# Kernel tuning notes

Hardware: AMD Instinct MI355X
Metric: run time of the kernel (lower is better)

Reference implementation:

```python
import jax, jax.numpy as jnp
import numpy as np

B, T, D, HD = 4, 4096, 1024, 64

def setup_inputs() -> dict:
    key = jax.random.key(0)
    k1, k2, k3, k4 = jax.random.split(key, 4)
    scale = 1.0 / np.sqrt(D)
    return {
        "x": jax.random.normal(k1, (B, T, D), dtype=jnp.float32),
        "Wq": jax.random.normal(k2, (HD, D), dtype=jnp.float32) * scale,
        "Wk": jax.random.normal(k3, (HD, D), dtype=jnp.float32) * scale,
        "Wv": jax.random.normal(k4, (HD, D), dtype=jnp.float32) * scale,
    }

def reference(x, Wq, Wk, Wv):
    # x: [B,T,D]; W*: [head_dim, D] (torch Linear weight layout)
    Q = jnp.einsum('btd,hd->bth', x, Wq)  # [B,T,HD]
    K = jnp.einsum('btd,hd->bth', x, Wk)
    V = jnp.einsum('btd,hd->bth', x, Wv)
    hd = Q.shape[-1]
    scores = jnp.einsum('bqh,bkh->bqk', Q, K) * (hd ** -0.5)  # [B,T,T]
    t = scores.shape[1]
    causal = jnp.tril(jnp.ones((t, t), dtype=bool))
    scores = jnp.where(causal, scores, -jnp.inf)
    att = jax.nn.softmax(scores, axis=-1)
    return jnp.einsum('bqk,bkh->bqh', att, V)  # [B,T,HD]
```

## Files before the change

### kernel.cpp

```cpp
#include <hip/hip_runtime.h>
#include <stdint.h>

#define B_  4
#define T_  4096
#define D_  1024
#define HD_ 64
#define BT_ 16384

typedef short bf16x8 __attribute__((ext_vector_type(8)));
typedef float f32x4  __attribute__((ext_vector_type(4)));
typedef float f32x16 __attribute__((ext_vector_type(16)));
typedef unsigned short u16;
typedef u16 u16x4 __attribute__((ext_vector_type(4)));
typedef unsigned int u32;
typedef u32 u32x4 __attribute__((ext_vector_type(4)));

#define M0L2_  11.54156032f
#define QSCALE_ 0.18033688f

#define CPB_   132
#define NSLOT_ (4 * CPB_ * 2)

__device__ __forceinline__ u16 f2bf(float f) {
    union { float f; unsigned u; } v; v.f = f;
    unsigned r = (v.u + 0x7FFF + ((v.u >> 16) & 1)) >> 16;
    return (u16)r;
}
__device__ __forceinline__ float bf2f(u16 u) {
    union { unsigned u; float f; } v; v.u = ((unsigned)u) << 16;
    return v.f;
}
__device__ __forceinline__ u32 cvt_pk_bf16(float lo, float hi) {
    u32 r;
    asm("v_cvt_pk_bf16_f32 %0, %1, %2" : "=v"(r) : "v"(lo), "v"(hi));
    return r;
}

__global__ __launch_bounds__(256) void wconv_kernel(
    const float* __restrict__ wq, const float* __restrict__ wk,
    const float* __restrict__ wv, u16* __restrict__ wb)
{
    const int j   = blockIdx.x >> 5;
    const int off = (blockIdx.x & 31) * 2048 + threadIdx.x * 8;
    const float* src = (j == 0) ? wq : ((j == 1) ? wk : wv);
    f32x4 a0 = *(const f32x4*)(src + off);
    f32x4 a1 = *(const f32x4*)(src + off + 4);
    u32x4 b;
    b[0] = cvt_pk_bf16(a0[0], a0[1]);
    b[1] = cvt_pk_bf16(a0[2], a0[3]);
    b[2] = cvt_pk_bf16(a1[0], a1[1]);
    b[3] = cvt_pk_bf16(a1[2], a1[3]);
    *(u32x4*)(wb + j * 65536 + off) = b;
}

struct StageSet { f32x4 xa, xb; bf16x8 w0, w1, w2; };

__global__ __launch_bounds__(512, 2) void qkv_kernel(
    const float* __restrict__ x, const u16* __restrict__ wb,
    u16* __restrict__ qs, u16* __restrict__ kss, u16* __restrict__ vssT)
{
    __shared__ __align__(16) u16 xt[2][64][72];
    __shared__ __align__(16) u16 wt[2][192][72];

    const int tid  = threadIdx.x;
    const int lane = tid & 63;
    const int w    = tid >> 6;
    const int quad = lane >> 4;
    const int l16  = lane & 15;
    const int row0 = blockIdx.x * 64;
    const int rh   = w >> 2;
    const int ct   = w & 3;

    const int xrow = tid >> 3;
    const int xcg  = tid & 7;

    f32x4 acc[2][3];
    #pragma unroll
    for (int s = 0; s < 2; ++s)
        #pragma unroll
        for (int g = 0; g < 3; ++g) acc[s][g] = (f32x4)0.0f;

    const float* xbase = x + (size_t)(row0 + xrow) * D_ + xcg * 8;

    auto load_tile = [&](StageSet& S, int t) {
        const float* xp = xbase + t * 64;
        S.xa = *(const f32x4*)xp; S.xb = *(const f32x4*)(xp + 4);
        const u16* wp = wb + t * 64;
        S.w0 = *(const bf16x8*)(wp + (size_t)((tid       ) >> 3) * D_ + ((tid       ) & 7) * 8);
        S.w1 = *(const bf16x8*)(wp + (size_t)((tid +  512) >> 3) * D_ + ((tid +  512) & 7) * 8);
        S.w2 = *(const bf16x8*)(wp + (size_t)((tid + 1024) >> 3) * D_ + ((tid + 1024) & 7) * 8);
    };
    auto store_tile = [&](const StageSet& S, int bufi) {
        u32x4 px;
        px[0] = cvt_pk_bf16(S.xa[0], S.xa[1]);
        px[1] = cvt_pk_bf16(S.xa[2], S.xa[3]);
        px[2] = cvt_pk_bf16(S.xb[0], S.xb[1]);
        px[3] = cvt_pk_bf16(S.xb[2], S.xb[3]);
        *(u32x4*)&xt[bufi][xrow][xcg * 8] = px;
        *(bf16x8*)&wt[bufi][(tid       ) >> 3][((tid       ) & 7) * 8] = S.w0;
        *(bf16x8*)&wt[bufi][(tid +  512) >> 3][((tid +  512) & 7) * 8] = S.w1;
        *(bf16x8*)&wt[bufi][(tid + 1024) >> 3][((tid + 1024) & 7) * 8] = S.w2;
    };
    auto compute = [&](int bufi) {
        #pragma unroll
        for (int ks = 0; ks < 2; ++ks) {
            bf16x8 a[2];
            #pragma unroll
            for (int s = 0; s < 2; ++s)
                a[s] = *(const bf16x8*)&xt[bufi][rh * 32 + s * 16 + l16][ks * 32 + quad * 8];
            #pragma unroll
            for (int g = 0; g < 3; ++g) {
                bf16x8 bfr = *(const bf16x8*)&wt[bufi][(ct * 3 + g) * 16 + l16][ks * 32 + quad * 8];
                #pragma unroll
                for (int s = 0; s < 2; ++s)
                    acc[s][g] = __builtin_amdgcn_mfma_f32_16x16x32_bf16(a[s], bfr, acc[s][g], 0, 0, 0);
            }
        }
    };

    StageSet A, B;
    load_tile(A, 0);
    load_tile(B, 1);
    store_tile(A, 0);
    __syncthreads();

    #pragma unroll
    for (int kc2 = 0; kc2 < 8; ++kc2) {
        const int kc = kc2 * 2;
        if (kc + 2 < 16) load_tile(A, kc + 2);
        compute(0);
        store_tile(B, 1);
        __syncthreads();
        if (kc + 3 < 16) load_tile(B, kc + 3);
        compute(1);
        if (kc + 2 < 16) store_tile(A, 0);
        __syncthreads();
    }

    #pragma unroll
    for (int s = 0; s < 2; ++s) {
        #pragma unroll
        for (int g = 0; g < 3; ++g) {
            const int n = (ct * 3 + g) * 16 + l16;
            const int j = n >> 6, h = n & 63;
            const int rbase = row0 + rh * 32 + s * 16 + quad * 4;
            if (j == 0) {
                #pragma unroll
                for (int r = 0; r < 4; ++r) qs[(size_t)(rbase + r) * HD_ + h] = f2bf(acc[s][g][r] * QSCALE_);
            } else if (j == 1) {
                #pragma unroll
                for (int r = 0; r < 4; ++r) kss[(size_t)(rbase + r) * HD_ + h] = f2bf(acc[s][g][r]);
            } else {
                u16x4 v;
                #pragma unroll
                for (int r = 0; r < 4; ++r) v[r] = f2bf(acc[s][g][r]);
                *(u16x4*)(vssT + (size_t)h * BT_ + rbase) = v;
            }
        }
    }
}

__global__ __launch_bounds__(256, 4) void attn_kernel(
    const u16* __restrict__ qs, const u16* __restrict__ kss,
    const u16* __restrict__ vssT,
    float* __restrict__ pl, u16* __restrict__ pO)
{
    __shared__ __align__(16) u16 kt2[8 * 65 * 8];
    __shared__ __align__(16) u16 vt2[8 * 65 * 8];

    const int m = blockIdx.x % CPB_;
    const int b = blockIdx.x / CPB_;

    int t0, bound, qtA, qtB;
    if (m < 120)      { int u = m >> 3; t0 = (m & 7) * 8; bound = 2 * u + 2; qtA = u;  qtB = 30 - u; }
    else if (m < 124) { t0 = (m - 120) * 8; bound = 1 << 30; qtA = 15; qtB = 15; }
    else              { t0 = (m - 124) * 8; bound = 1 << 30; qtA = 31; qtB = 31; }

    const int tid  = threadIdx.x;
    const int lane = tid & 63;
    const int w    = tid >> 6;
    const int l31  = lane & 31;
    const int hi   = lane >> 5;
    const size_t base = (size_t)b * T_;

    int qt    = (t0 < bound) ? qtA : qtB;
    int kti   = (t0 < bound) ? t0 : (t0 - bound);
    int qrow0 = qt * 128 + w * 32;

    bf16x8 qf[4];
    #pragma unroll
    for (int ds = 0; ds < 4; ++ds)
        qf[ds] = *(const bf16x8*)(qs + (base + qrow0 + l31) * HD_ + ds * 16 + hi * 8);

    f32x16 o0 = (f32x16)0.0f, o1 = (f32x16)0.0f;
    float l_acc = 0.0f;

    const int srow = tid >> 2, q4 = tid & 3;
    const u16* kp = kss  + (base + srow) * HD_ + q4 * 16;
    const u16* vp = vssT + (size_t)srow * BT_ + base + q4 * 16;
    u16* kdst = kt2 + ((((srow >> 5) * 4 + q4) * 65 + (srow & 31)) * 8);
    u16* vdst = vt2 + ((((srow >> 5) * 4 + q4) * 65 + (srow & 31)) * 8);

    bf16x8 kr0, kr1, vr0, vr1;
    {
        const u16* k0 = kp + (size_t)kti * 64 * HD_;
        kr0 = *(const bf16x8*)k0; kr1 = *(const bf16x8*)(k0 + 8);
        const u16* v0 = vp + kti * 64;
        vr0 = *(const bf16x8*)v0; vr1 = *(const bf16x8*)(v0 + 8);
    }

    auto FLUSH = [&](int role) {
        const int slot = (b * CPB_ + m) * 2 + role;
        u32 la = __builtin_bit_cast(u32, l_acc), lb = la;
        asm("v_permlane32_swap_b32 %0, %1" : "+v"(la), "+v"(lb));
        float lfull = __builtin_bit_cast(float, la) + __builtin_bit_cast(float, lb);
        if (hi == 0) pl[slot * 128 + w * 32 + l31] = lfull;
        #pragma unroll
        for (int reg = 0; reg < 16; ++reg) {
            int row = w * 32 + (reg & 3) + 8 * (reg >> 2) + 4 * hi;
            pO[(size_t)slot * 8192 + row * 64 + l31]      = f2bf(o0[reg]);
            pO[(size_t)slot * 8192 + row * 64 + 32 + l31] = f2bf(o1[reg]);
        }
    };

    for (int step = 0; step < 8; ++step) {
        const int i = t0 + step;
        __syncthreads();
        *(bf16x8*)(kdst)       = kr0;
        *(bf16x8*)(kdst + 256) = kr1;
        *(bf16x8*)(vdst)       = vr0;
        *(bf16x8*)(vdst + 256) = vr1;
        __syncthreads();

        int kti_next = 0;
        if (step < 7) {
            kti_next = (i + 1 < bound) ? (i + 1) : (i + 1 - bound);
            const u16* k0 = kp + (size_t)kti_next * 64 * HD_;
            kr0 = *(const bf16x8*)k0; kr1 = *(const bf16x8*)(k0 + 8);
            const u16* v0 = vp + kti_next * 64;
            vr0 = *(const bf16x8*)v0; vr1 = *(const bf16x8*)(v0 + 8);
        }

        if (kti * 64 <= qrow0 + 31) {
            const bool diag = (kti * 64 + 63 > qrow0);
            const int  qa   = qrow0 + l31;
            u32 wv[16];
            #pragma unroll
            for (int kg = 0; kg < 2; ++kg) {
                f32x16 s = (f32x16)0.0f;
                __builtin_amdgcn_s_setprio(1);
                #pragma unroll
                for (int ds = 0; ds < 4; ++ds) {
                    bf16x8 af = *(const bf16x8*)(kt2 + ((kg * 4 + ds) * 65 + lane) * 8);
                    s = __builtin_amdgcn_mfma_f32_32x32x16_bf16(af, qf[ds], s, 0, 0, 0);
                }
                __builtin_amdgcn_s_setprio(0);
                float lp = 0.0f;
                #pragma unroll
                for (int rp = 0; rp < 8; ++rp) {
                    float e0 = __builtin_amdgcn_exp2f(s[2 * rp]     - M0L2_);
                    float e1 = __builtin_amdgcn_exp2f(s[2 * rp + 1] - M0L2_);
                    if (diag) {
                        const int k0e = kti * 64 + kg * 32 + ((2 * rp) & 3) + 8 * ((2 * rp) >> 2) + 4 * hi;
                        if (k0e > qa)     e0 = 0.0f;
                        if (k0e + 1 > qa) e1 = 0.0f;
                    }
                    lp += e0 + e1;
                    wv[kg * 8 + rp] = cvt_pk_bf16(e0, e1);
                }
                l_acc += lp;
            }
            bf16x8 pa[4];
            #pragma unroll
            for (int ks = 0; ks < 4; ++ks) {
                const int kg2 = ks >> 1, k1 = ks & 1;
                u32 x0 = wv[kg2 * 8 + k1 * 4 + 0], y0 = wv[kg2 * 8 + k1 * 4 + 2];
                u32 x1 = wv[kg2 * 8 + k1 * 4 + 1], y1 = wv[kg2 * 8 + k1 * 4 + 3];
                asm("v_permlane32_swap_b32 %0, %1" : "+v"(x0), "+v"(y0));
                asm("v_permlane32_swap_b32 %0, %1" : "+v"(x1), "+v"(y1));
                u32x4 t; t[0] = x0; t[1] = x1; t[2] = y0; t[3] = y1;
                pa[ks] = __builtin_bit_cast(bf16x8, t);
            }
            __builtin_amdgcn_s_setprio(1);
            #pragma unroll
            for (int ks = 0; ks < 4; ++ks) {
                bf16x8 vf0 = *(const bf16x8*)(vt2 + ((0 * 4 + ks) * 65 + lane) * 8);
                o0 = __builtin_amdgcn_mfma_f32_32x32x16_bf16(pa[ks], vf0, o0, 0, 0, 0);
                bf16x8 vf1 = *(const bf16x8*)(vt2 + ((1 * 4 + ks) * 65 + lane) * 8);
                o1 = __builtin_amdgcn_mfma_f32_32x32x16_bf16(pa[ks], vf1, o1, 0, 0, 0);
            }
            __builtin_amdgcn_s_setprio(0);
        }

        kti = kti_next;
        if (step < 7 && (i + 1) == bound) {
            FLUSH(0);
            o0 = (f32x16)0.0f; o1 = (f32x16)0.0f; l_acc = 0.0f;
            qt = qtB; qrow0 = qt * 128 + w * 32;
            #pragma unroll
            for (int ds = 0; ds < 4; ++ds)
                qf[ds] = *(const bf16x8*)(qs + (base + qrow0 + l31) * HD_ + ds * 16 + hi * 8);
        }
    }
    FLUSH((t0 + 7 >= bound) ? 1 : 0);
}

__global__ __launch_bounds__(256) void merge_kernel(
    const float* __restrict__ pl, const u16* __restrict__ pO,
    float* __restrict__ out)
{
    const int bi  = blockIdx.x;
    const int rh  = bi & 1;
    const int qt2 = (bi >> 1) & 31;
    const int b   = bi >> 6;

    int c0, c1, role, mbase;
    if (qt2 <= 14)      { int u = qt2;      c0 = 0;                c1 = (2 * u + 1) >> 3; role = 0; mbase = u * 8; }
    else if (qt2 == 15) { c0 = 0;           c1 = 3;                role = 0; mbase = 120; }
    else if (qt2 <= 30) { int u = 30 - qt2; c0 = (2 * u + 2) >> 3; c1 = 7;  role = 1; mbase = u * 8; }
    else                { c0 = 0;           c1 = 7;                role = 0; mbase = 124; }

    const int row = rh * 64 + (threadIdx.x >> 2);
    const int hg  = (threadIdx.x & 3) * 16;

    float L = 0.0f;
    float o[16];
    #pragma unroll
    for (int i = 0; i < 16; ++i) o[i] = 0.0f;
    for (int c = c0; c <= c1; ++c) {
        const int slot = (b * CPB_ + mbase + c) * 2 + role;
        L += pl[slot * 128 + row];
        const u16* p = pO + (size_t)slot * 8192 + row * 64 + hg;
        bf16x8 v0 = *(const bf16x8*)p;
        bf16x8 v1 = *(const bf16x8*)(p + 8);
        #pragma unroll
        for (int i = 0; i < 8; ++i) { o[i] += bf2f((u16)v0[i]); o[8 + i] += bf2f((u16)v1[i]); }
    }
    const float inv = 1.0f / L;
    float* op = out + ((size_t)b * T_ + qt2 * 128 + row) * HD_ + hg;
    #pragma unroll
    for (int j = 0; j < 4; ++j) {
        f32x4 v;
        #pragma unroll
        for (int i = 0; i < 4; ++i) v[i] = o[j * 4 + i] * inv;
        *(f32x4*)(op + j * 4) = v;
    }
}

extern "C" void kernel_launch(void* const* d_in, const int* in_sizes, int n_in,
                              void* d_out, int out_size, void* d_ws, size_t ws_size,
                              hipStream_t stream) {
    const float* x  = (const float*)d_in[0];
    const float* wq = (const float*)d_in[1];
    const float* wk = (const float*)d_in[2];
    const float* wv = (const float*)d_in[3];

    const size_t NE = (size_t)BT_ * HD_;
    char* ws = (char*)d_ws;
    u16* qs   = (u16*)ws;
    u16* kss  = qs  + NE;
    u16* vssT = kss + NE;
    u16* wb   = vssT + NE;
    float* pl = (float*)(wb + 192 * 1024);
    u16* pO   = (u16*)(pl + (size_t)NSLOT_ * 128);
    float* out = (float*)d_out;

    wconv_kernel<<<dim3(96),        dim3(256), 0, stream>>>(wq, wk, wv, wb);
    qkv_kernel  <<<dim3(256),       dim3(512), 0, stream>>>(x, wb, qs, kss, vssT);
    attn_kernel <<<dim3(4 * CPB_),  dim3(256), 0, stream>>>(qs, kss, vssT, pl, pO);
    merge_kernel<<<dim3(256),       dim3(256), 0, stream>>>(pl, pO, out);
}
```

Measured before the change: 146.1 us.

## Load QKV weight tiles straight into LDS with a pre-swizzled layout

The weight-conversion kernel now writes bf16 weights in an XOR-swizzled 16-byte-chunk layout. The QKV projection kernel then copies each weight tile straight from global memory into LDS with global_load_lds, instead of staging it through registers and storing it to LDS. The compute loop reads B fragments using the matching XOR index, which is meant to avoid LDS bank conflicts and to free registers and VALU store instructions. The double-buffer loop is simplified to a single rolled loop with one barrier per k-step. This depends on the barrier waiting for the asynchronous LDS DMA, and the rolled loop may cost some scheduling freedom.

```diff
diff --git a/kernel.cpp b/kernel.cpp
--- a/kernel.cpp
+++ b/kernel.cpp
@@ -35,32 +35,39 @@
     asm("v_cvt_pk_bf16_f32 %0, %1, %2" : "=v"(r) : "v"(lo), "v"(hi));
     return r;
 }
+__device__ __forceinline__ void gload_lds16(const void* g, void* l) {
+    __builtin_amdgcn_global_load_lds(
+        (const __attribute__((address_space(1))) unsigned int*)g,
+        (__attribute__((address_space(3))) unsigned int*)l, 16, 0, 0);
+}
 
 __global__ __launch_bounds__(256) void wconv_kernel(
     const float* __restrict__ wq, const float* __restrict__ wk,
     const float* __restrict__ wv, u16* __restrict__ wb)
 {
-    const int j   = blockIdx.x >> 5;
-    const int off = (blockIdx.x & 31) * 2048 + threadIdx.x * 8;
-    const float* src = (j == 0) ? wq : ((j == 1) ? wk : wv);
-    f32x4 a0 = *(const f32x4*)(src + off);
-    f32x4 a1 = *(const f32x4*)(src + off + 4);
+    const int cid = blockIdx.x * 256 + threadIdx.x;
+    const int n   = cid >> 7;
+    const int kg  = cid & 127;
+    const int mat = n >> 6, row = n & 63;
+    const float* src = (mat == 0) ? wq : ((mat == 1) ? wk : wv);
+    const float* p = src + row * 1024 + kg * 8;
+    f32x4 a0 = *(const f32x4*)p;
+    f32x4 a1 = *(const f32x4*)(p + 4);
     u32x4 b;
     b[0] = cvt_pk_bf16(a0[0], a0[1]);
     b[1] = cvt_pk_bf16(a0[2], a0[3]);
     b[2] = cvt_pk_bf16(a1[0], a1[1]);
     b[3] = cvt_pk_bf16(a1[2], a1[3]);
-    *(u32x4*)(wb + j * 65536 + off) = b;
-}
-
-struct StageSet { f32x4 xa, xb; bf16x8 w0, w1, w2; };
+    const int dkg = (kg & ~7) | ((kg & 7) ^ (n & 7));
+    *(u32x4*)(wb + ((size_t)n * 128 + dkg) * 8) = b;
+}
 
 __global__ __launch_bounds__(512, 2) void qkv_kernel(
     const float* __restrict__ x, const u16* __restrict__ wb,
     u16* __restrict__ qs, u16* __restrict__ kss, u16* __restrict__ vssT)
 {
     __shared__ __align__(16) u16 xt[2][64][72];
-    __shared__ __align__(16) u16 wt[2][192][72];
+    __shared__ __align__(16) u16 wt[2][1536 * 8];
 
     const int tid  = threadIdx.x;
     const int lane = tid & 63;
@@ -82,24 +89,38 @@
 
     const float* xbase = x + (size_t)(row0 + xrow) * D_ + xcg * 8;
 
-    auto load_tile = [&](StageSet& S, int t) {
+    const u16* wsrc[3];
+    u16* wdst[3];
+    #pragma unroll
+    for (int i = 0; i < 3; ++i) {
+        const int c = tid + 512 * i;
+        wsrc[i] = wb + (size_t)c * 8 * 16;
+        wdst[i] = (u16*)wt + (size_t)c * 8;
+    }
+    #pragma unroll
+    for (int i = 0; i < 3; ++i) {
+        const int c = tid + 512 * i;
+        const int n = c >> 3, cg = c & 7;
+        wsrc[i] = wb + ((size_t)n * 128 + cg) * 8;
+    }
+
+    f32x4 xa, xb;
+    auto xload = [&](int t) {
         const float* xp = xbase + t * 64;
-        S.xa = *(const f32x4*)xp; S.xb = *(const f32x4*)(xp + 4);
-        const u16* wp = wb + t * 64;
-        S.w0 = *(const bf16x8*)(wp + (size_t)((tid       ) >> 3) * D_ + ((tid       ) & 7) * 8);
-        S.w1 = *(const bf16x8*)(wp + (size_t)((tid +  512) >> 3) * D_ + ((tid +  512) & 7) * 8);
-        S.w2 = *(const bf16x8*)(wp + (size_t)((tid + 1024) >> 3) * D_ + ((tid + 1024) & 7) * 8);
-    };
-    auto store_tile = [&](const StageSet& S, int bufi) {
+        xa = *(const f32x4*)xp; xb = *(const f32x4*)(xp + 4);
+    };
+    auto xstore = [&](int bufi) {
         u32x4 px;
-        px[0] = cvt_pk_bf16(S.xa[0], S.xa[1]);
-        px[1] = cvt_pk_bf16(S.xa[2], S.xa[3]);
-        px[2] = cvt_pk_bf16(S.xb[0], S.xb[1]);
-        px[3] = cvt_pk_bf16(S.xb[2], S.xb[3]);
+        px[0] = cvt_pk_bf16(xa[0], xa[1]);
+        px[1] = cvt_pk_bf16(xa[2], xa[3]);
+        px[2] = cvt_pk_bf16(xb[0], xb[1]);
+        px[3] = cvt_pk_bf16(xb[2], xb[3]);
         *(u32x4*)&xt[bufi][xrow][xcg * 8] = px;
-        *(bf16x8*)&wt[bufi][(tid       ) >> 3][((tid       ) & 7) * 8] = S.w0;
-        *(bf16x8*)&wt[bufi][(tid +  512) >> 3][((tid +  512) & 7) * 8] = S.w1;
-        *(bf16x8*)&wt[bufi][(tid + 1024) >> 3][((tid + 1024) & 7) * 8] = S.w2;
+    };
+    auto wload = [&](int t, int bufi) {
+        #pragma unroll
+        for (int i = 0; i < 3; ++i)
+            gload_lds16(wsrc[i] + t * 64, wdst[i] + bufi * 12288);
     };
     auto compute = [&](int bufi) {
         #pragma unroll
@@ -110,7 +131,8 @@
                 a[s] = *(const bf16x8*)&xt[bufi][rh * 32 + s * 16 + l16][ks * 32 + quad * 8];
             #pragma unroll
             for (int g = 0; g < 3; ++g) {
-                bf16x8 bfr = *(const bf16x8*)&wt[bufi][(ct * 3 + g) * 16 + l16][ks * 32 + quad * 8];
+                const int n = (ct * 3 + g) * 16 + l16;
+                bf16x8 bfr = *(const bf16x8*)&wt[bufi][n * 64 + ((ks * 32 + quad * 8) ^ ((l16 & 7) * 8))];
                 #pragma unroll
                 for (int s = 0; s < 2; ++s)
                     acc[s][g] = __builtin_amdgcn_mfma_f32_16x16x32_bf16(a[s], bfr, acc[s][g], 0, 0, 0);
@@ -118,22 +140,19 @@
         }
     };
 
-    StageSet A, B;
-    load_tile(A, 0);
-    load_tile(B, 1);
-    store_tile(A, 0);
+    xload(0);
+    wload(0, 0);
+    xstore(0);
     __syncthreads();
 
-    #pragma unroll
-    for (int kc2 = 0; kc2 < 8; ++kc2) {
-        const int kc = kc2 * 2;
-        if (kc + 2 < 16) load_tile(A, kc + 2);
-        compute(0);
-        store_tile(B, 1);
-        __syncthreads();
-        if (kc + 3 < 16) load_tile(B, kc + 3);
-        compute(1);
-        if (kc + 2 < 16) store_tile(A, 0);
+    for (int kc = 0; kc < 16; ++kc) {
+        const int cur = kc & 1;
+        if (kc < 15) {
+            wload(kc + 1, cur ^ 1);
+            xload(kc + 1);
+        }
+        compute(cur);
+        if (kc < 15) xstore(cur ^ 1);
         __syncthreads();
     }
 
```

Result: no change. 145.5 us (-0.4%).
